# Optimization experiments

Hardware: AMD Instinct MI355X
Metric: run time of the kernel (lower is better)

Reference implementation:

```python
import jax, jax.numpy as jnp
import numpy as np
from jax import lax

B = 8192
HS = 64        # hidden_size (output channels)
HS4 = HS + 4   # internal channel count (68)
K = 3          # conv kernel size


def setup_inputs() -> dict:
    key = jax.random.key(0)
    ks = jax.random.split(key, 16)
    def n(k, shape, s=1.0):
        return jax.random.normal(k, shape, dtype=jnp.float32) * s
    return {
        "x": n(ks[0], (B, HS, 6, 6)),
        "cell": n(ks[1], (B, 2)),
        "interspace_coord": n(ks[2], (B, 2, 6, 6)),
        "conv1_w": n(ks[3], (HS4, HS4, K, K), 0.05),
        "conv1_b": n(ks[4], (HS4,), 0.05),
        "conv3_w": n(ks[5], (HS4, HS4, K, K), 0.05),
        "conv3_b": n(ks[6], (HS4,), 0.05),
        "lin5_w": n(ks[7], (9 * HS, HS4 * 25), 0.02),
        "lin5_b": n(ks[8], (9 * HS,), 0.02),
        "lin4_w": n(ks[9], (9 * HS, HS4 * 16), 0.02),
        "lin4_b": n(ks[10], (9 * HS,), 0.02),
        "lin3_w": n(ks[11], (9 * HS, HS4 * 9), 0.02),
        "lin3_b": n(ks[12], (9 * HS,), 0.02),
        "final_w": n(ks[13], (HS, 9 * HS), 0.02),
        "final_b": n(ks[14], (HS,), 0.02),
    }


def _conv(z, w, b):
    # torch Conv2d with padding=k//2, stride 1 == SAME conv, NCHW/OIHW
    y = lax.conv_general_dilated(z, w, (1, 1), 'SAME',
                                 dimension_numbers=('NCHW', 'OIHW', 'NCHW'))
    return y + b[None, :, None, None]


def _corners(z, ws):
    # four corner windows, stacked on a new leading axis (corner-major)
    H, W = z.shape[-2:]
    return jnp.stack([z[..., :ws, :ws],
                      z[..., :ws, W - ws:],
                      z[..., H - ws:, :ws],
                      z[..., H - ws:, W - ws:]], axis=0)


def reference(x, cell, interspace_coord,
              conv1_w, conv1_b, conv3_w, conv3_b,
              lin5_w, lin5_b, lin4_w, lin4_b, lin3_w, lin3_b,
              final_w, final_b):
    Bn = x.shape[0]
    new_cell = jnp.broadcast_to(cell.reshape(Bn, -1)[:, :, None, None],
                                (Bn, 2, 6, 6))
    lins = {5: (lin5_w, lin5_b), 4: (lin4_w, lin4_b), 3: (lin3_w, lin3_b)}
    for ws in (5, 4, 3):
        z = jnp.concatenate([x, new_cell, interspace_coord], axis=1)  # [B,68,6,6]
        z = _corners(z, ws).reshape(-1, HS4, ws, ws)                  # [4B,68,ws,ws]
        z = jnp.sin(z) + jnp.cos(z)
        z = jax.nn.relu(_conv(z, conv1_w, conv1_b))
        z = jnp.sin(z) + jnp.cos(z)
        z = jax.nn.relu(_conv(z, conv3_w, conv3_b)).reshape(4, Bn, -1)
        Wl, bl = lins[ws]
        z = jax.nn.relu(z @ Wl.T + bl).reshape(4, Bn, HS, 3, 3)
        m = jnp.concatenate([z[0], z[1]], axis=-1)   # [B,64,3,6]
        n = jnp.concatenate([z[2], z[3]], axis=-1)
        x = jnp.concatenate([m, n], axis=-2)          # [B,64,6,6]
    ew = 3
    c = _corners(x, ew)                               # [4,B,64,3,3]
    c = c.reshape(4 * Bn, -1) @ final_w.T + final_b   # [4B,64]
    c = c.reshape(Bn, HS, 2, 2)                       # same flat-order reshape as torch
    xc = x[:, :, ew - 1:ew + 1, ew - 1:ew + 1]        # center 2x2
    return (xc * c).reshape(Bn, HS, -1)
```

## Files before the change

### kernel.cpp

```cpp
#include <hip/hip_runtime.h>
#include <hip/hip_bf16.h>
#include <cstdint>
#include <cstddef>

#define BN 8192
#define MTOT 32768

using bf16 = __hip_bfloat16;
typedef float f32x4 __attribute__((ext_vector_type(4)));
typedef short short8 __attribute__((ext_vector_type(8)));

__device__ __forceinline__ bf16 f2b(float v) { return __float2bfloat16(v); }
__device__ __forceinline__ float b2f(bf16 v) { return __bfloat162float(v); }
__device__ __forceinline__ float sincos_sum(float x) {
    return 1.41421356237f * __sinf(x + 0.78539816340f);
}


__global__ __launch_bounds__(256)
void zprep_block(const float* __restrict__ xF, const float* __restrict__ cell,
                 const float* __restrict__ isc, bf16* __restrict__ Z,
                 int m0g, int CM)
{
    constexpr int KD = 1728, KTRUE = 1700;
    const int b = blockIdx.x, tid = threadIdx.x;
    __shared__ float s[68][37];

    for (int i = tid; i < 64 * 36; i += 256) {
        int ic = i / 36, off = i % 36;
        s[ic][off] = sincos_sum(xF[((size_t)b * 64 + ic) * 36 + off]);
    }
    if (tid < 2) {
        float t = sincos_sum(cell[b * 2 + tid]);
        #pragma unroll
        for (int off = 0; off < 36; off++) s[64 + tid][off] = t;
    }
    if (tid >= 64 && tid < 136) {
        int j = tid - 64;
        int ic = j / 36, off = j % 36;
        s[66 + ic][off] = sincos_sum(isc[((size_t)b * 2 + ic) * 36 + off]);
    }
    __syncthreads();

    for (int i = tid; i < 4 * (KD / 8); i += 256) {
        int q = i / (KD / 8), j8 = i % (KD / 8);
        int gm = q * BN + b;
        if (gm < m0g || gm >= m0g + CM) continue;
        int kbase = j8 * 8;
        short8 pack;
        #pragma unroll
        for (int u = 0; u < 8; u++) {
            int k = kbase + u;
            float v = 0.f;
            if (k < KTRUE) {
                int pi = k / 68, ic = k % 68;
                int r = (q >> 1) + pi / 5;
                int c = (q & 1) + pi % 5;
                v = s[ic][r * 6 + c];
            }
            bf16 bv = f2b(v);
            pack[u] = *reinterpret_cast<short*>(&bv);
        }
        *reinterpret_cast<short8*>(&Z[(size_t)(gm - m0g) * KD + kbase]) = pack;
    }
}

template<int WSv>
__device__ __forceinline__ bf16 conv_elem(const float* __restrict__ src, int n, int k)
{
    constexpr int KTRUE = 68 * WSv * WSv;
    float v = 0.f;
    if (n < KTRUE && k < KTRUE) {
        int po = n / 68, oc = n % 68, ro = po / WSv, co = po % WSv;
        int pi = k / 68, ic = k % 68, ri = pi / WSv, ci = pi % WSv;
        int kr = ri - ro + 1, kc = ci - co + 1;
        if (kr >= 0 && kr < 3 && kc >= 0 && kc < 3)
            v = src[((oc * 68 + ic) * 3 + kr) * 3 + kc];
    }
    return f2b(v);
}
template<int WSv>
__device__ __forceinline__ bf16 lin_elem(const float* __restrict__ wl, int n, int k)
{
    constexpr int KTRUE = 68 * WSv * WSv;
    float v = 0.f;
    if (n < 576 && k < KTRUE) {
        int pi = k / 68, ic = k % 68;
        v = wl[(size_t)n * KTRUE + ic * (WSv * WSv) + pi];
    }
    return f2b(v);
}

__global__ void megabuild(const float* __restrict__ c1w, const float* __restrict__ c3w,
                          const float* __restrict__ l5w, const float* __restrict__ l4w,
                          const float* __restrict__ l3w, const float* __restrict__ fw,
                          const float* __restrict__ c1b, const float* __restrict__ c3b,
                          const float* __restrict__ bl5, const float* __restrict__ bl4,
                          const float* __restrict__ bl3, const float* __restrict__ bfin,
                          const float* __restrict__ cell, const float* __restrict__ isc,
                          bf16* __restrict__ w1d5, bf16* __restrict__ w3d5,
                          bf16* __restrict__ w1d4, bf16* __restrict__ w3d4,
                          bf16* __restrict__ w1d3, bf16* __restrict__ w3d3,
                          bf16* __restrict__ wl5p, bf16* __restrict__ wl4p,
                          bf16* __restrict__ wl3p, bf16* __restrict__ wfp,
                          float* __restrict__ bias,
                          bf16* __restrict__ Z4, bf16* __restrict__ Z3)
{
    constexpr unsigned S0 = 2u*1792*1728, S1 = 2u*1152*1088, S2 = 2u*640*640;
    constexpr unsigned S3 = 640u*1728, S4 = 640u*1088, S5 = 640u*640;
    constexpr unsigned S6 = 128u*576, S7 = 9216;
    constexpr unsigned S8 = 4u*8192*16*4, S9 = 4u*8192*9*4, S10 = 32768u*28;
    constexpr unsigned O1=S0, O2=O1+S1, O3=O2+S2, O4=O3+S3, O5=O4+S4, O6=O5+S5,
                       O7=O6+S6, O8=O7+S7, O9=O8+S8, O10=O9+S9, OT=O10+S10;
    unsigned e = blockIdx.x * 256u + threadIdx.x;
    if (e >= OT) return;
    if (e < O1) {
        constexpr unsigned per = 1792u*1728;
        unsigned i = (e < per) ? e : e - per;
        bf16* dst = (e < per) ? w1d5 : w3d5;
        const float* src = (e < per) ? c1w : c3w;
        dst[i] = conv_elem<5>(src, (int)(i / 1728u), (int)(i % 1728u));
    } else if (e < O2) {
        unsigned i0 = e - O1; constexpr unsigned per = 1152u*1088;
        unsigned i = (i0 < per) ? i0 : i0 - per;
        bf16* dst = (i0 < per) ? w1d4 : w3d4;
        const float* src = (i0 < per) ? c1w : c3w;
        dst[i] = conv_elem<4>(src, (int)(i / 1088u), (int)(i % 1088u));
    } else if (e < O3) {
        unsigned i0 = e - O2; constexpr unsigned per = 640u*640;
        unsigned i = (i0 < per) ? i0 : i0 - per;
        bf16* dst = (i0 < per) ? w1d3 : w3d3;
        const float* src = (i0 < per) ? c1w : c3w;
        dst[i] = conv_elem<3>(src, (int)(i / 640u), (int)(i % 640u));
    } else if (e < O4) {
        unsigned i = e - O3;
        wl5p[i] = lin_elem<5>(l5w, (int)(i / 1728u), (int)(i % 1728u));
    } else if (e < O5) {
        unsigned i = e - O4;
        wl4p[i] = lin_elem<4>(l4w, (int)(i / 1088u), (int)(i % 1088u));
    } else if (e < O6) {
        unsigned i = e - O5;
        wl3p[i] = lin_elem<3>(l3w, (int)(i / 640u), (int)(i % 640u));
    } else if (e < O7) {
        unsigned i = e - O6, n = i / 576u, k = i % 576u;
        wfp[i] = (n < 64u) ? f2b(fw[n * 576u + k]) : f2b(0.f);
    } else if (e < O8) {
        int i = (int)(e - O7);
        float v = 0.f;
        if (i < 1792)      { int n = i;        if (n < 1700) v = c1b[n % 68]; }
        else if (i < 3584) { int n = i - 1792; if (n < 1700) v = c3b[n % 68]; }
        else if (i < 4736) { int n = i - 3584; if (n < 1088) v = c1b[n % 68]; }
        else if (i < 5888) { int n = i - 4736; if (n < 1088) v = c3b[n % 68]; }
        else if (i < 6528) { int n = i - 5888; if (n < 612)  v = c1b[n % 68]; }
        else if (i < 7168) { int n = i - 6528; if (n < 612)  v = c3b[n % 68]; }
        else if (i < 7808) { int n = i - 7168; if (n < 576)  v = bl5[n]; }
        else if (i < 8448) { int n = i - 7808; if (n < 576)  v = bl4[n]; }
        else if (i < 9088) { int n = i - 8448; if (n < 576)  v = bl3[n]; }
        else               { int n = i - 9088; if (n < 64)   v = bfin[n]; }
        bias[i] = v;
    } else if (e < O9) {
        unsigned i = e - O8;
        int j = (int)(i & 3u); i >>= 2;
        int pi = (int)(i & 15u); i >>= 4;
        int b = (int)(i & 8191u); int q = (int)(i >> 13);
        float t;
        if (j < 2) t = cell[b * 2 + j];
        else {
            int r = (q >> 1) * 2 + pi / 4, c = (q & 1) * 2 + pi % 4;
            t = isc[((size_t)b * 2 + (j - 2)) * 36 + r * 6 + c];
        }
        Z4[((size_t)q * BN + b) * 1088 + pi * 68 + 64 + j] = f2b(sincos_sum(t));
    } else if (e < O10) {
        unsigned i = e - O9;
        int j = (int)(i & 3u); i >>= 2;
        int pi = (int)(i % 9u); i /= 9u;
        int b = (int)(i & 8191u); int q = (int)(i >> 13);
        float t;
        if (j < 2) t = cell[b * 2 + j];
        else {
            int r = (q >> 1) * 3 + pi / 3, c = (q & 1) * 3 + pi % 3;
            t = isc[((size_t)b * 2 + (j - 2)) * 36 + r * 6 + c];
        }
        Z3[((size_t)q * BN + b) * 640 + pi * 68 + 64 + j] = f2b(sincos_sum(t));
    } else {
        unsigned i = e - O10;
        int m = (int)(i / 28u), t = (int)(i % 28u);
        Z3[(size_t)m * 640 + 612 + t] = f2b(0.f);
    }
}

__device__ __forceinline__ void gload_lds16(const bf16* g, const bf16* lds_wave_base)
{
    unsigned off = (unsigned)(uintptr_t)lds_wave_base;
    off = __builtin_amdgcn_readfirstlane(off);
    __builtin_amdgcn_global_load_lds((const __attribute__((address_space(1))) unsigned int*)g,
                                     (__attribute__((address_space(3))) unsigned int*)off,
                                     16, 0, 0);
}

__device__ __forceinline__ int imin(int a, int b) { return a < b ? a : b; }
__device__ __forceinline__ int imax(int a, int b) { return a > b ? a : b; }

template<int EPI, int WS, int WN, int WIDE>
__global__ __launch_bounds__(512, 4)
void gemm8(const bf16* __restrict__ A, const bf16* __restrict__ Bm, int KD,
           const float* __restrict__ bias, int ntiles, int mtiles,
           bf16* __restrict__ C, int ldc, int nlimit,
           int m0g, bf16* __restrict__ znext)
{
    constexpr int BMc = WIDE ? 128 : 256;
    constexpr int BNc = WIDE ? 256 : 128;
    constexpr int NWN = WIDE ? 4 : 2;
    __shared__ bf16 As[3][BMc * 32];
    __shared__ bf16 Bs[3][BNc * 32];
    const int tid = threadIdx.x;
    const int wave = tid >> 6, lane = tid & 63;
    const int l15 = lane & 15, lq = lane >> 4;
    const int wr = (wave / NWN) * 64, wc = (wave % NWN) * 64;

    const int xcd = blockIdx.x & 7, lblk = blockIdx.x >> 3;
    const int bpx = (int)gridDim.x >> 3;
    const int mloc = mtiles >> 3;
    const int tot = mloc * ntiles;

    const int srow = tid >> 2;
    const int scx = (tid & 3) ^ ((srow >> 1) & 3);
    const int sOff = srow * 32 + (tid & 3) * 8;
    const int swz = (lq ^ ((l15 >> 1) & 3)) * 8;
    const int offA0 = (wr + l15) * 32 + swz;
    const int offB0 = (wc + l15) * 32 + swz;

    for (int w = lblk; w < tot; w += bpx) {
        const int m_idx = (w / ntiles) * 8 + xcd;
        const int n_idx = w % ntiles;
        const int n0 = n_idx * BNc, m0 = m_idx * BMc;

        int s0b = 0, s0e = KD, s1b = 0, s1e = 0, s2b = 0, s2e = 0;
        if (WS > 0) {
            int po_lo = imin(n0 / 68, WS * WS - 1);
            int po_hi = imin((n0 + BNc - 1) / 68, WS * WS - 1);
            int ro_lo = po_lo / WS, ro_hi = po_hi / WS;
            int r_lo = imax(ro_lo - 1, 0), r_hi = imin(ro_hi + 1, WS - 1);
            int ci_lo = 0, ci_hi = WS - 1;
            if (ro_lo == ro_hi) {
                ci_lo = imax(po_lo % WS - 1, 0);
                ci_hi = imin(po_hi % WS + 1, WS - 1);
            }
            if (ci_lo == 0 && ci_hi == WS - 1) {
                s0b = (r_lo * WS * 68) & ~31;
                s0e = imin(KD, ((r_hi + 1) * WS * 68 + 31) & ~31);
            } else {
                s0b = ((r_lo * WS + ci_lo) * 68) & ~31;
                s0e = imin(KD, (((r_lo * WS + ci_hi + 1) * 68) + 31) & ~31);
                if (r_hi > r_lo) {
                    s1b = (((r_lo + 1) * WS + ci_lo) * 68) & ~31;
                    s1e = imin(KD, ((((r_lo + 1) * WS + ci_hi + 1) * 68) + 31) & ~31);
                }
                if (r_hi > r_lo + 1) {
                    s2b = (((r_lo + 2) * WS + ci_lo) * 68) & ~31;
                    s2e = imin(KD, ((((r_lo + 2) * WS + ci_hi + 1) * 68) + 31) & ~31);
                }
            }
        }
        const int c0 = (s0e - s0b) >> 5;
        const int c1 = c0 + ((s1e - s1b) >> 5);
        const int nt = c1 + ((s2e - s2b) >> 5);
        auto k0_of = [&](int t2) -> int {
            int k = s0b + (t2 << 5);
            if (t2 >= c0) k = s1b + ((t2 - c0) << 5);
            if (t2 >= c1) k = s2b + ((t2 - c1) << 5);
            return k;
        };

        const bf16* aSrc = A + (size_t)(m0 + srow) * KD + scx * 8;
        const bf16* bSrc = Bm + (size_t)(n0 + srow) * KD + scx * 8;

        auto stageAll = [&](int k0, int buf) {
            if (WIDE) {
                gload_lds16(aSrc + k0, &As[buf][sOff]);
                gload_lds16(bSrc + k0, &Bs[buf][sOff]);
                gload_lds16(bSrc + k0 + (size_t)128 * KD, &Bs[buf][sOff + 4096]);
            } else {
                gload_lds16(aSrc + k0, &As[buf][sOff]);
                gload_lds16(aSrc + k0 + (size_t)128 * KD, &As[buf][sOff + 4096]);
                gload_lds16(bSrc + k0, &Bs[buf][sOff]);
            }
        };

        f32x4 acc[4][4];
        #pragma unroll
        for (int i = 0; i < 4; i++)
            #pragma unroll
            for (int j = 0; j < 4; j++) { f32x4 z = {0.f, 0.f, 0.f, 0.f}; acc[i][j] = z; }

        {
            stageAll(k0_of(0), 0);
            if (nt > 1) stageAll(k0_of(1), 1);
            __syncthreads();
        }

        for (int t = 0; t < nt; ++t) {
            const int cur = t % 3;
            const int nx = (t + 2) % 3;
            const bool pf = (t + 2) < nt;

            const bf16* Ac = &As[cur][0];
            const bf16* Bc = &Bs[cur][0];

            short8 af[4], bg[4];
            #pragma unroll
            for (int i = 0; i < 4; i++) af[i] = *(const short8*)&Ac[offA0 + i * 512];
            #pragma unroll
            for (int j = 0; j < 4; j++) bg[j] = *(const short8*)&Bc[offB0 + j * 512];

            if (pf) stageAll(k0_of(t + 2), nx);

            __builtin_amdgcn_s_setprio(1);
            #pragma unroll
            for (int i = 0; i < 4; i++)
                #pragma unroll
                for (int j = 0; j < 4; j++)
                    acc[i][j] = __builtin_amdgcn_mfma_f32_16x16x32_bf16(af[i], bg[j], acc[i][j], 0, 0, 0);
            __builtin_amdgcn_s_setprio(0);

            if (pf) asm volatile("s_waitcnt vmcnt(3)" ::: "memory");
            else    asm volatile("s_waitcnt vmcnt(0)" ::: "memory");
            __builtin_amdgcn_s_barrier();
        }

        float bj[4];
        #pragma unroll
        for (int j = 0; j < 4; j++) bj[j] = bias[n0 + wc + j * 16 + l15];

        #pragma unroll
        for (int i = 0; i < 4; i++) {
            #pragma unroll
            for (int j = 0; j < 4; j++) {
                int n = n0 + wc + j * 16 + l15;
                #pragma unroll
                for (int r = 0; r < 4; r++) {
                    int m = m0 + wr + i * 16 + lq * 4 + r;
                    float v = acc[i][j][r];
                    if (EPI == 0) {
                        if (n < nlimit) {
                            v += bj[j]; v = fmaxf(v, 0.f); v = sincos_sum(v);
                            C[(size_t)m * ldc + n] = f2b(v);
                        }
                    } else if (EPI == 1) {
                        if (n < nlimit) {
                            v += bj[j]; v = fmaxf(v, 0.f);
                            C[(size_t)m * ldc + n] = f2b(v);
                        }
                    } else {
                        if (n < 576) {
                            v += bj[j]; v = fmaxf(v, 0.f);
                            bf16 tv = f2b(sincos_sum(v));
                            int gm = m0g + m;
                            int q = gm >> 13, b = gm & (BN - 1);
                            int ch = n / 9, p = n % 9;
                            int R = p / 3 + (q >> 1) * 3, Cc = p % 3 + (q & 1) * 3;
                            constexpr int OFF = 6 - WN;
                            constexpr int KDN = (WN == 4) ? 1088 : 640;
                            #pragma unroll
                            for (int qr = 0; qr < 2; qr++) {
                                int rr = R - OFF * qr;
                                if (rr < 0 || rr >= WN) continue;
                                #pragma unroll
                                for (int qc = 0; qc < 2; qc++) {
                                    int cc = Cc - OFF * qc;
                                    if (cc < 0 || cc >= WN) continue;
                                    int pi = rr * WN + cc;
                                    znext[((size_t)((qr * 2 + qc) * BN + b)) * KDN + pi * 68 + ch] = tv;
                                }
                            }
                        }
                    }
                }
            }
        }
    }
}

template<int EPI, int WS, int WN>
__global__ __launch_bounds__(256)
void gemm_bt(const bf16* __restrict__ A, const bf16* __restrict__ Bm, int KD,
             const float* __restrict__ bias, int ntiles,
             bf16* __restrict__ C, int ldc, int nlimit,
             int m0g, bf16* __restrict__ znext,
             const bf16* __restrict__ afin_xc, float* __restrict__ outp)
{
    __shared__ bf16 As[128 * 32];
    __shared__ bf16 Bs[128 * 32];
    const int tid = threadIdx.x;
    const int wave = tid >> 6, lane = tid & 63;
    const int l15 = lane & 15, lq = lane >> 4;
    const int wr = (wave >> 1) * 64, wc = (wave & 1) * 64;

    const int id = blockIdx.x;
    const int mt8 = (int)gridDim.x / (ntiles * 8);
    const int xcd = id & 7, local = id >> 3;
    const int m_idx = xcd * mt8 + local / ntiles;
    const int n_idx = local % ntiles;
    const int n0 = n_idx * 128, m0 = m_idx * 128;

    int nspans = 1, sbeg[4], send[4];
    sbeg[0] = 0; send[0] = KD;
    if (WS > 0) {
        int po_lo = imin(n0 / 68, WS * WS - 1);
        int po_hi = imin((n0 + 127) / 68, WS * WS - 1);
        int ro_lo = po_lo / WS, ro_hi = po_hi / WS;
        int r_lo = imax(ro_lo - 1, 0), r_hi = imin(ro_hi + 1, WS - 1);
        int ci_lo = 0, ci_hi = WS - 1;
        if (ro_lo == ro_hi) {
            ci_lo = imax(po_lo % WS - 1, 0);
            ci_hi = imin(po_hi % WS + 1, WS - 1);
        }
        if (ci_lo == 0 && ci_hi == WS - 1) {
            sbeg[0] = (r_lo * WS * 68) & ~31;
            send[0] = imin(KD, ((r_hi + 1) * WS * 68 + 31) & ~31);
        } else {
            nspans = 0;
            for (int ri = r_lo; ri <= r_hi; ri++) {
                sbeg[nspans] = ((ri * WS + ci_lo) * 68) & ~31;
                send[nspans] = imin(KD, (((ri * WS + ci_hi + 1) * 68) + 31) & ~31);
                nspans++;
            }
        }
    }

    float bj[4];
    #pragma unroll
    for (int j = 0; j < 4; j++) bj[j] = bias[n0 + wc + j * 16 + l15];

    const bf16* Ab = A + (size_t)m0 * KD;
    const bf16* Bb = Bm + (size_t)n0 * KD;
    const int srow = tid >> 2, scol = (tid & 3) * 8;
    const bf16* aG0 = Ab + (size_t)srow * KD + scol;
    const bf16* aG1 = Ab + (size_t)(srow + 64) * KD + scol;
    const bf16* bG0 = Bb + (size_t)srow * KD + scol;
    const bf16* bG1 = Bb + (size_t)(srow + 64) * KD + scol;
    const bf16* lA0 = &As[wave * 512];
    const bf16* lA1 = &As[2048 + wave * 512];
    const bf16* lB0 = &Bs[wave * 512];
    const bf16* lB1 = &Bs[2048 + wave * 512];

    f32x4 acc[4][4];
    #pragma unroll
    for (int i = 0; i < 4; i++)
        #pragma unroll
        for (int j = 0; j < 4; j++) { f32x4 z = {0.f, 0.f, 0.f, 0.f}; acc[i][j] = z; }

    for (int s = 0; s < nspans; s++) {
        for (int k0 = sbeg[s]; k0 < send[s]; k0 += 32) {
            gload_lds16(aG0 + k0, lA0);
            gload_lds16(aG1 + k0, lA1);
            gload_lds16(bG0 + k0, lB0);
            gload_lds16(bG1 + k0, lB1);
            __syncthreads();
            short8 af[4], bg[4];
            #pragma unroll
            for (int i = 0; i < 4; i++) af[i] = *(const short8*)&As[(wr + i * 16 + l15) * 32 + lq * 8];
            #pragma unroll
            for (int j = 0; j < 4; j++) bg[j] = *(const short8*)&Bs[(wc + j * 16 + l15) * 32 + lq * 8];
            #pragma unroll
            for (int i = 0; i < 4; i++)
                #pragma unroll
                for (int j = 0; j < 4; j++)
                    acc[i][j] = __builtin_amdgcn_mfma_f32_16x16x32_bf16(af[i], bg[j], acc[i][j], 0, 0, 0);
            __syncthreads();
        }
    }

    #pragma unroll
    for (int i = 0; i < 4; i++) {
        #pragma unroll
        for (int j = 0; j < 4; j++) {
            int n = n0 + wc + j * 16 + l15;
            #pragma unroll
            for (int r = 0; r < 4; r++) {
                int m = m0 + wr + i * 16 + lq * 4 + r;
                float v = acc[i][j][r];
                if (EPI == 0) {
                    if (n < nlimit) {
                        v += bj[j]; v = fmaxf(v, 0.f); v = sincos_sum(v);
                        C[(size_t)m * ldc + n] = f2b(v);
                    }
                } else if (EPI == 1) {
                    if (n < nlimit) {
                        v += bj[j]; v = fmaxf(v, 0.f);
                        C[(size_t)m * ldc + n] = f2b(v);
                    }
                } else if (EPI == 2) {
                    if (n < 576) {
                        v += bj[j]; v = fmaxf(v, 0.f);
                        bf16 t = f2b(sincos_sum(v));
                        int gm = m0g + m;
                        int q = gm >> 13, b = gm & (BN - 1);
                        int ch = n / 9, p = n % 9;
                        int R = p / 3 + (q >> 1) * 3, Cc = p % 3 + (q & 1) * 3;
                        constexpr int OFF = 6 - WN;
                        constexpr int KDN = (WN == 4) ? 1088 : 640;
                        #pragma unroll
                        for (int qr = 0; qr < 2; qr++) {
                            int rr = R - OFF * qr;
                            if (rr < 0 || rr >= WN) continue;
                            #pragma unroll
                            for (int qc = 0; qc < 2; qc++) {
                                int cc = Cc - OFF * qc;
                                if (cc < 0 || cc >= WN) continue;
                                int pi = rr * WN + cc;
                                znext[((size_t)((qr * 2 + qc) * BN + b)) * KDN + pi * 68 + ch] = t;
                            }
                        }
                    }
                } else {
                    if (n < 64) {
                        v += bj[j];
                        int gm = m0g + m;
                        int f = gm * 64 + n;
                        int b2 = f >> 8, rem = f & 255;
                        int ch2 = rem >> 2, ii = (rem >> 1) & 1, jj = rem & 1;
                        int qq = ii * 2 + jj;
                        const int offt[4] = {8, 6, 2, 0};
                        float xc = b2f(afin_xc[((size_t)qq * BN + b2) * 576 + ch2 * 9 + offt[qq]]);
                        outp[f] = v * xc;
                    }
                }
            }
        }
    }
}

extern "C" void kernel_launch(void* const* d_in, const int* in_sizes, int n_in,
                              void* d_out, int out_size, void* d_ws, size_t ws_size,
                              hipStream_t stream)
{
    const float* x    = (const float*)d_in[0];
    const float* cell = (const float*)d_in[1];
    const float* isc  = (const float*)d_in[2];
    const float* c1w  = (const float*)d_in[3];
    const float* c1b  = (const float*)d_in[4];
    const float* c3w  = (const float*)d_in[5];
    const float* c3b  = (const float*)d_in[6];
    const float* l5w  = (const float*)d_in[7];
    const float* l5b  = (const float*)d_in[8];
    const float* l4w  = (const float*)d_in[9];
    const float* l4b  = (const float*)d_in[10];
    const float* l3w  = (const float*)d_in[11];
    const float* l3b  = (const float*)d_in[12];
    const float* fw   = (const float*)d_in[13];
    const float* fb   = (const float*)d_in[14];

    char* base = (char*)d_ws;
    size_t cur = 0;
    auto take = [&](size_t bytes) -> char* {
        char* r = base + cur; cur += (bytes + 255) & ~(size_t)255; return r;
    };

    const size_t Z4B = (size_t)MTOT * 1088 * 2;
    const size_t Z3B = (size_t)MTOT * 640 * 2;
    const size_t AFB = (size_t)MTOT * 576 * 2;
    size_t wbytes = 2 * (1792ull * 1728 + 1152ull * 1088 + 640ull * 640) * 2
                  + (640ull * 1728 + 640ull * 1088 + 640ull * 640) * 2
                  + 128ull * 576 * 2 + 9216ull * 4 + 64 * 256;
    auto need = [&](int nc) -> size_t {
        return Z4B + Z3B + AFB + wbytes + 2 * ((size_t)(MTOT / nc) * 1728 * 2);
    };
    int nchunk = (ws_size >= need(1)) ? 1 : (ws_size >= need(2)) ? 2
               : (ws_size >= need(4)) ? 4 : (ws_size >= need(8)) ? 8 : 16;

    bf16* Z4   = (bf16*)take(Z4B);
    bf16* Z3   = (bf16*)take(Z3B);
    bf16* afinb = (bf16*)take(AFB);
    bf16* w1d5 = (bf16*)take(1792ull * 1728 * 2);
    bf16* w3d5 = (bf16*)take(1792ull * 1728 * 2);
    bf16* w1d4 = (bf16*)take(1152ull * 1088 * 2);
    bf16* w3d4 = (bf16*)take(1152ull * 1088 * 2);
    bf16* w1d3 = (bf16*)take(640ull * 640 * 2);
    bf16* w3d3 = (bf16*)take(640ull * 640 * 2);
    bf16* wl5p = (bf16*)take(640ull * 1728 * 2);
    bf16* wl4p = (bf16*)take(640ull * 1088 * 2);
    bf16* wl3p = (bf16*)take(640ull * 640 * 2);
    bf16* wfp  = (bf16*)take(128ull * 576 * 2);
    float* biasb = (float*)take(9216ull * 4);
    int CM = MTOT / nchunk;
    int mt = CM / 128;
    int mt2 = CM / 256;
    bf16* Za = (bf16*)take((size_t)CM * 1728 * 2);
    bf16* Zb = (bf16*)take((size_t)CM * 1728 * 2);

    {
        constexpr unsigned OT = 2u*1792*1728 + 2u*1152*1088 + 2u*640*640
                              + 640u*1728 + 640u*1088 + 640u*640 + 128u*576 + 9216
                              + 4u*8192*16*4 + 4u*8192*9*4 + 32768u*28;
        megabuild<<<(OT + 255) / 256, 256, 0, stream>>>(
            c1w, c3w, l5w, l4w, l3w, fw, c1b, c3b, l5b, l4b, l3b, fb, cell, isc,
            w1d5, w3d5, w1d4, w3d4, w1d3, w3d3, wl5p, wl4p, wl3p, wfp, biasb, Z4, Z3);
    }

    for (int c = 0; c < nchunk; c++) {
        int m0g = c * CM;
        zprep_block<<<BN, 256, 0, stream>>>(x, cell, isc, Za, m0g, CM);
        gemm8<0, 5, 0, 1><<<512, 512, 0, stream>>>(Za, w1d5, 1728, biasb + 0, 7, mt,
                                                   Zb, 1728, 1728, 0, nullptr);
        gemm8<1, 5, 0, 1><<<512, 512, 0, stream>>>(Zb, w3d5, 1728, biasb + 1792, 7, mt,
                                                   Za, 1728, 1728, 0, nullptr);
        gemm8<2, 0, 4, 0><<<512, 512, 0, stream>>>(Za, wl5p, 1728, biasb + 7168, 5, mt2,
                                                   nullptr, 0, 0, m0g, Z4);
    }
    for (int c = 0; c < nchunk; c++) {
        int m0g = c * CM;
        gemm8<0, 4, 0, 0><<<512, 512, 0, stream>>>(Z4 + (size_t)m0g * 1088, w1d4, 1088,
                                                   biasb + 3584, 9, mt2, Zb, 1088, 1088,
                                                   0, nullptr);
        gemm8<1, 4, 0, 0><<<512, 512, 0, stream>>>(Zb, w3d4, 1088, biasb + 4736, 9, mt2,
                                                   Za, 1088, 1088, 0, nullptr);
        gemm8<2, 0, 3, 0><<<512, 512, 0, stream>>>(Za, wl4p, 1088, biasb + 7808, 5, mt2,
                                                   nullptr, 0, 0, m0g, Z3);
    }
    for (int c = 0; c < nchunk; c++) {
        int m0g = c * CM;
        gemm8<0, 3, 0, 0><<<512, 512, 0, stream>>>(Z3 + (size_t)m0g * 640, w1d3, 640,
                                                   biasb + 5888, 5, mt2, Zb, 640, 640,
                                                   0, nullptr);
        gemm8<1, 3, 0, 0><<<512, 512, 0, stream>>>(Zb, w3d3, 640, biasb + 6528, 5, mt2,
                                                   Za, 640, 640, 0, nullptr);
        gemm8<1, 0, 0, 0><<<512, 512, 0, stream>>>(Za, wl3p, 640, biasb + 8448, 5, mt2,
                                                   afinb + (size_t)m0g * 576, 576, 576,
                                                   0, nullptr);
    }
    for (int c = 0; c < nchunk; c++) {
        int m0g = c * CM;
        gemm_bt<3, 0, 0><<<mt, 256, 0, stream>>>(afinb + (size_t)m0g * 576, wfp, 576,
                                                 biasb + 9088, 1, nullptr, 0, 0, m0g,
                                                 nullptr, afinb, (float*)d_out);
    }
}
```

Measured before the change: 1.243 ms.

## Load A fragments directly to registers and shrink GEMM tile to 128x128

Replaces the 512-thread GEMM with a 256-thread 128x128-tile kernel. Only B is staged through LDS with triple buffering. Each wave loads its A fragments straight from global memory into registers, prefetched one K step ahead. This removes the A LDS traffic and cuts LDS footprint so more blocks fit, at the cost of uncoalesced global reads for A and more tiles (more B re-reads). Launch grids change to 768 blocks.

```diff
diff --git a/kernel.cpp b/kernel.cpp
--- a/kernel.cpp
+++ b/kernel.cpp
@@ -201,22 +201,18 @@
 __device__ __forceinline__ int imin(int a, int b) { return a < b ? a : b; }
 __device__ __forceinline__ int imax(int a, int b) { return a > b ? a : b; }
 
-template<int EPI, int WS, int WN, int WIDE>
-__global__ __launch_bounds__(512, 4)
-void gemm8(const bf16* __restrict__ A, const bf16* __restrict__ Bm, int KD,
+template<int EPI, int WS, int WN>
+__global__ __launch_bounds__(256, 3)
+void gemm9(const bf16* __restrict__ A, const bf16* __restrict__ Bm, int KD,
            const float* __restrict__ bias, int ntiles, int mtiles,
            bf16* __restrict__ C, int ldc, int nlimit,
            int m0g, bf16* __restrict__ znext)
 {
-    constexpr int BMc = WIDE ? 128 : 256;
-    constexpr int BNc = WIDE ? 256 : 128;
-    constexpr int NWN = WIDE ? 4 : 2;
-    __shared__ bf16 As[3][BMc * 32];
-    __shared__ bf16 Bs[3][BNc * 32];
+    __shared__ bf16 Bs[3][4096];
     const int tid = threadIdx.x;
     const int wave = tid >> 6, lane = tid & 63;
     const int l15 = lane & 15, lq = lane >> 4;
-    const int wr = (wave / NWN) * 64, wc = (wave % NWN) * 64;
+    const int wr = (wave >> 1) * 64, wc = (wave & 1) * 64;
 
     const int xcd = blockIdx.x & 7, lblk = blockIdx.x >> 3;
     const int bpx = (int)gridDim.x >> 3;
@@ -227,18 +223,17 @@
     const int scx = (tid & 3) ^ ((srow >> 1) & 3);
     const int sOff = srow * 32 + (tid & 3) * 8;
     const int swz = (lq ^ ((l15 >> 1) & 3)) * 8;
-    const int offA0 = (wr + l15) * 32 + swz;
     const int offB0 = (wc + l15) * 32 + swz;
 
     for (int w = lblk; w < tot; w += bpx) {
         const int m_idx = (w / ntiles) * 8 + xcd;
         const int n_idx = w % ntiles;
-        const int n0 = n_idx * BNc, m0 = m_idx * BMc;
+        const int n0 = n_idx * 128, m0 = m_idx * 128;
 
         int s0b = 0, s0e = KD, s1b = 0, s1e = 0, s2b = 0, s2e = 0;
         if (WS > 0) {
             int po_lo = imin(n0 / 68, WS * WS - 1);
-            int po_hi = imin((n0 + BNc - 1) / 68, WS * WS - 1);
+            int po_hi = imin((n0 + 127) / 68, WS * WS - 1);
             int ro_lo = po_lo / WS, ro_hi = po_hi / WS;
             int r_lo = imax(ro_lo - 1, 0), r_hi = imin(ro_hi + 1, WS - 1);
             int ci_lo = 0, ci_hi = WS - 1;
@@ -272,20 +267,16 @@
             return k;
         };
 
-        const bf16* aSrc = A + (size_t)(m0 + srow) * KD + scx * 8;
         const bf16* bSrc = Bm + (size_t)(n0 + srow) * KD + scx * 8;
-
-        auto stageAll = [&](int k0, int buf) {
-            if (WIDE) {
-                gload_lds16(aSrc + k0, &As[buf][sOff]);
-                gload_lds16(bSrc + k0, &Bs[buf][sOff]);
-                gload_lds16(bSrc + k0 + (size_t)128 * KD, &Bs[buf][sOff + 4096]);
-            } else {
-                gload_lds16(aSrc + k0, &As[buf][sOff]);
-                gload_lds16(aSrc + k0 + (size_t)128 * KD, &As[buf][sOff + 4096]);
-                gload_lds16(bSrc + k0, &Bs[buf][sOff]);
-            }
+        auto stageB = [&](int k0, int buf) {
+            gload_lds16(bSrc + k0, &Bs[buf][sOff]);
+            gload_lds16(bSrc + k0 + (size_t)64 * KD, &Bs[buf][sOff + 2048]);
         };
+
+        const bf16* aR0 = A + (size_t)(m0 + wr +  0 + l15) * KD + lq * 8;
+        const bf16* aR1 = A + (size_t)(m0 + wr + 16 + l15) * KD + lq * 8;
+        const bf16* aR2 = A + (size_t)(m0 + wr + 32 + l15) * KD + lq * 8;
+        const bf16* aR3 = A + (size_t)(m0 + wr + 48 + l15) * KD + lq * 8;
 
         f32x4 acc[4][4];
         #pragma unroll
@@ -293,38 +284,52 @@
             #pragma unroll
             for (int j = 0; j < 4; j++) { f32x4 z = {0.f, 0.f, 0.f, 0.f}; acc[i][j] = z; }
 
+        short8 afC[4], afN[4];
         {
-            stageAll(k0_of(0), 0);
-            if (nt > 1) stageAll(k0_of(1), 1);
+            const int k0a = k0_of(0);
+            afC[0] = *(const short8*)(aR0 + k0a);
+            afC[1] = *(const short8*)(aR1 + k0a);
+            afC[2] = *(const short8*)(aR2 + k0a);
+            afC[3] = *(const short8*)(aR3 + k0a);
+            stageB(k0a, 0);
+            if (nt > 1) stageB(k0_of(1), 1);
             __syncthreads();
         }
 
         for (int t = 0; t < nt; ++t) {
             const int cur = t % 3;
             const int nx = (t + 2) % 3;
-            const bool pf = (t + 2) < nt;
-
-            const bf16* Ac = &As[cur][0];
-            const bf16* Bc = &Bs[cur][0];
-
-            short8 af[4], bg[4];
-            #pragma unroll
-            for (int i = 0; i < 4; i++) af[i] = *(const short8*)&Ac[offA0 + i * 512];
-            #pragma unroll
-            for (int j = 0; j < 4; j++) bg[j] = *(const short8*)&Bc[offB0 + j * 512];
-
-            if (pf) stageAll(k0_of(t + 2), nx);
+            const bool pfA = (t + 1) < nt;
+            const bool pfB = (t + 2) < nt;
+
+            short8 bg[4];
+            #pragma unroll
+            for (int j = 0; j < 4; j++) bg[j] = *(const short8*)&Bs[cur][offB0 + j * 512];
+
+            if (pfA) {
+                const int kA = k0_of(t + 1);
+                afN[0] = *(const short8*)(aR0 + kA);
+                afN[1] = *(const short8*)(aR1 + kA);
+                afN[2] = *(const short8*)(aR2 + kA);
+                afN[3] = *(const short8*)(aR3 + kA);
+            }
+            if (pfB) stageB(k0_of(t + 2), nx);
 
             __builtin_amdgcn_s_setprio(1);
             #pragma unroll
             for (int i = 0; i < 4; i++)
                 #pragma unroll
                 for (int j = 0; j < 4; j++)
-                    acc[i][j] = __builtin_amdgcn_mfma_f32_16x16x32_bf16(af[i], bg[j], acc[i][j], 0, 0, 0);
+                    acc[i][j] = __builtin_amdgcn_mfma_f32_16x16x32_bf16(afC[i], bg[j], acc[i][j], 0, 0, 0);
             __builtin_amdgcn_s_setprio(0);
 
-            if (pf) asm volatile("s_waitcnt vmcnt(3)" ::: "memory");
-            else    asm volatile("s_waitcnt vmcnt(0)" ::: "memory");
+            if (pfA) {
+                #pragma unroll
+                for (int i = 0; i < 4; i++) afC[i] = afN[i];
+            }
+
+            if (pfB)      asm volatile("s_waitcnt vmcnt(6)" ::: "memory");
+            else if (pfA) asm volatile("s_waitcnt vmcnt(4)" ::: "memory");
             __builtin_amdgcn_s_barrier();
         }
 
@@ -585,7 +590,6 @@
     float* biasb = (float*)take(9216ull * 4);
     int CM = MTOT / nchunk;
     int mt = CM / 128;
-    int mt2 = CM / 256;
     bf16* Za = (bf16*)take((size_t)CM * 1728 * 2);
     bf16* Zb = (bf16*)take((size_t)CM * 1728 * 2);
 
@@ -601,33 +605,33 @@
     for (int c = 0; c < nchunk; c++) {
         int m0g = c * CM;
         zprep_block<<<BN, 256, 0, stream>>>(x, cell, isc, Za, m0g, CM);
-        gemm8<0, 5, 0, 1><<<512, 512, 0, stream>>>(Za, w1d5, 1728, biasb + 0, 7, mt,
-                                                   Zb, 1728, 1728, 0, nullptr);
-        gemm8<1, 5, 0, 1><<<512, 512, 0, stream>>>(Zb, w3d5, 1728, biasb + 1792, 7, mt,
-                                                   Za, 1728, 1728, 0, nullptr);
-        gemm8<2, 0, 4, 0><<<512, 512, 0, stream>>>(Za, wl5p, 1728, biasb + 7168, 5, mt2,
-                                                   nullptr, 0, 0, m0g, Z4);
+        gemm9<0, 5, 0><<<768, 256, 0, stream>>>(Za, w1d5, 1728, biasb + 0, 14, mt,
+                                                Zb, 1728, 1728, 0, nullptr);
+        gemm9<1, 5, 0><<<768, 256, 0, stream>>>(Zb, w3d5, 1728, biasb + 1792, 14, mt,
+                                                Za, 1728, 1728, 0, nullptr);
+        gemm9<2, 0, 4><<<768, 256, 0, stream>>>(Za, wl5p, 1728, biasb + 7168, 5, mt,
+                                                nullptr, 0, 0, m0g, Z4);
     }
     for (int c = 0; c < nchunk; c++) {
         int m0g = c * CM;
-        gemm8<0, 4, 0, 0><<<512, 512, 0, stream>>>(Z4 + (size_t)m0g * 1088, w1d4, 1088,
-                                                   biasb + 3584, 9, mt2, Zb, 1088, 1088,
-                                                   0, nullptr);
-        gemm8<1, 4, 0, 0><<<512, 512, 0, stream>>>(Zb, w3d4, 1088, biasb + 4736, 9, mt2,
-                                                   Za, 1088, 1088, 0, nullptr);
-        gemm8<2, 0, 3, 0><<<512, 512, 0, stream>>>(Za, wl4p, 1088, biasb + 7808, 5, mt2,
-                                                   nullptr, 0, 0, m0g, Z3);
+        gemm9<0, 4, 0><<<768, 256, 0, stream>>>(Z4 + (size_t)m0g * 1088, w1d4, 1088,
+                                                biasb + 3584, 9, mt, Zb, 1088, 1088,
+                                                0, nullptr);
+        gemm9<1, 4, 0><<<768, 256, 0, stream>>>(Zb, w3d4, 1088, biasb + 4736, 9, mt,
+                                                Za, 1088, 1088, 0, nullptr);
+        gemm9<2, 0, 3><<<768, 256, 0, stream>>>(Za, wl4p, 1088, biasb + 7808, 5, mt,
+                                                nullptr, 0, 0, m0g, Z3);
     }
     for (int c = 0; c < nchunk; c++) {
         int m0g = c * CM;
-        gemm8<0, 3, 0, 0><<<512, 512, 0, stream>>>(Z3 + (size_t)m0g * 640, w1d3, 640,
-                                                   biasb + 5888, 5, mt2, Zb, 640, 640,
-                                                   0, nullptr);
-        gemm8<1, 3, 0, 0><<<512, 512, 0, stream>>>(Zb, w3d3, 640, biasb + 6528, 5, mt2,
-                                                   Za, 640, 640, 0, nullptr);
-        gemm8<1, 0, 0, 0><<<512, 512, 0, stream>>>(Za, wl3p, 640, biasb + 8448, 5, mt2,
-                                                   afinb + (size_t)m0g * 576, 576, 576,
-                                                   0, nullptr);
+        gemm9<0, 3, 0><<<768, 256, 0, stream>>>(Z3 + (size_t)m0g * 640, w1d3, 640,
+                                                biasb + 5888, 5, mt, Zb, 640, 640,
+                                                0, nullptr);
+        gemm9<1, 3, 0><<<768, 256, 0, stream>>>(Zb, w3d3, 640, biasb + 6528, 5, mt,
+                                                Za, 640, 640, 0, nullptr);
+        gemm9<1, 0, 0><<<768, 256, 0, stream>>>(Za, wl3p, 640, biasb + 8448, 5, mt,
+                                                afinb + (size_t)m0g * 576, 576, 576,
+                                                0, nullptr);
     }
     for (int c = 0; c < nchunk; c++) {
         int m0g = c * CM;
```

Result: slower. 1.800 ms (+44.9%).
